# Kernel optimization log

Hardware: AMD Instinct MI355X
Metric: run time of the kernel (lower is better)

Reference implementation:

```python
import jax, jax.numpy as jnp
import numpy as np

HEADS = 16
SEQ_LEN = 2048
EMB = 1024
BATCH = 2


def setup_inputs() -> dict:
    key = jax.random.key(0)
    ks = jax.random.split(key, 5)
    s = 1.0 / np.sqrt(EMB)
    return {
        "x": jax.random.normal(ks[0], (BATCH, SEQ_LEN, EMB), dtype=jnp.float32),
        "Wk": jax.random.normal(ks[1], (EMB, EMB), dtype=jnp.float32) * s,
        "Wq": jax.random.normal(ks[2], (EMB, EMB), dtype=jnp.float32) * s,
        "Wv": jax.random.normal(ks[3], (EMB, EMB), dtype=jnp.float32) * s,
        "Wu": jax.random.normal(ks[4], (EMB, EMB), dtype=jnp.float32) * s,
        "bu": jnp.zeros((EMB,), dtype=jnp.float32),
    }


def reference(x, Wk, Wq, Wv, Wu, bu):
    B, S, E = x.shape
    H = HEADS
    D = E // H
    # projections (torch Linear: y = x @ W.T); split heads -> [B, H, S, D]
    def proj(W):
        return (x @ W.T).reshape(B, S, H, D).transpose(0, 2, 1, 3)
    q, k, v = proj(Wq), proj(Wk), proj(Wv)
    scores = jnp.einsum("bhsd,bhtd->bhst", q, k) / jnp.sqrt(jnp.float32(D))
    causal_mask = jnp.triu(jnp.ones((S, S), dtype=bool), k=1)  # True above diag
    scores = jnp.where(causal_mask, -jnp.inf, scores)
    attn = jax.nn.softmax(scores, axis=-1)
    ctx = jnp.einsum("bhst,bhtd->bhsd", attn, v)  # [B,H,S,D]
    out = ctx.transpose(0, 2, 1, 3).reshape(B, S, E)
    return out @ Wu.T + bu
```

## Files before the change

### kernel.cpp

```cpp
#include <hip/hip_runtime.h>
#include <hip/hip_bf16.h>

#define HEADS 16
#define SEQ   2048
#define EMB   1024
#define BATCH 2
#define DHEAD 64
#define MTOK  (BATCH * SEQ)

typedef __bf16 bf16x8 __attribute__((ext_vector_type(8)));
typedef float  floatx4 __attribute__((ext_vector_type(4)));

__device__ __forceinline__ void gl_lds16(const void* g, void* l) {
  __builtin_amdgcn_global_load_lds((__attribute__((address_space(1))) void*)(g),
                                   (__attribute__((address_space(3))) void*)(l), 16, 0, 0);
}

__device__ __forceinline__ unsigned short f2bf(float f) {
  __bf16 h = (__bf16)f;
  return __builtin_bit_cast(unsigned short, h);
}

__global__ __launch_bounds__(256) void cvt_kernel(
    const float* __restrict__ x,  const float* __restrict__ wq,
    const float* __restrict__ wk, const float* __restrict__ wv,
    const float* __restrict__ wu,
    unsigned short* __restrict__ xb,  unsigned short* __restrict__ wqb,
    unsigned short* __restrict__ wkb, unsigned short* __restrict__ wvb,
    unsigned short* __restrict__ wub) {
  const int g = blockIdx.x * 256 + threadIdx.x;
  const int XG = (MTOK * EMB) / 4;
  const int WG = (EMB * EMB) / 4;
  const float* src; unsigned short* dst; int off;
  if (g < XG) { src = x; dst = xb; off = g; }
  else {
    int t = g - XG; int wsel = t / WG; off = t - wsel * WG;
    const float* ss[4] = {wq, wk, wv, wu};
    unsigned short* dd[4] = {wqb, wkb, wvb, wub};
    src = ss[wsel]; dst = dd[wsel];
  }
  float4 v = ((const float4*)src)[off];
  ushort4 o;
  o.x = f2bf(v.x); o.y = f2bf(v.y); o.z = f2bf(v.z); o.w = f2bf(v.w);
  ((ushort4*)dst)[off] = o;
}

__global__ __launch_bounds__(256) void gemm_qkv(
    const unsigned short* __restrict__ xb,
    const unsigned short* __restrict__ wqb, const unsigned short* __restrict__ wkb,
    const unsigned short* __restrict__ wvb,
    unsigned short* __restrict__ Qb, unsigned short* __restrict__ Kb,
    unsigned short* __restrict__ Vt) {
  constexpr int BM = 128, BN = 64, BK = 64;
  __shared__ unsigned short As[BM * BK];
  __shared__ unsigned short Bs[3 * BN * BK];
  const int m0 = blockIdx.x * BM, n0 = blockIdx.y * BN;
  const int tid = threadIdx.x, w = tid >> 6, lane = tid & 63;
  const int quad = lane >> 4, l16 = lane & 15;
  const int wm = w >> 1, wn = w & 1;
  const int srow = lane >> 3;
  const int scol = ((lane & 7) ^ srow) * 8;
  const unsigned short* Ws[3] = {wqb, wkb, wvb};

  floatx4 acc[3][4][2] = {};

  for (int kt = 0; kt < EMB / BK; ++kt) {
    const int k0 = kt * BK;
#pragma unroll
    for (int i = 0; i < 4; ++i) {
      int r0 = i * 32 + w * 8;
      gl_lds16(xb + (size_t)(m0 + r0 + srow) * EMB + k0 + scol, &As[r0 * BK]);
    }
#pragma unroll
    for (int z = 0; z < 3; ++z)
#pragma unroll
      for (int i = 0; i < 2; ++i) {
        int r0 = i * 32 + w * 8;
        gl_lds16(Ws[z] + (size_t)(n0 + r0 + srow) * EMB + k0 + scol,
                 &Bs[z * (BN * BK) + r0 * BK]);
      }
    __syncthreads();
#pragma unroll
    for (int ks = 0; ks < 2; ++ks) {
      bf16x8 af[4];
#pragma unroll
      for (int mb = 0; mb < 4; ++mb) {
        int ra = wm * 64 + mb * 16 + l16;
        af[mb] = *(const bf16x8*)&As[ra * BK + (((ks * 4 + quad) ^ (ra & 7)) * 8)];
      }
#pragma unroll
      for (int z = 0; z < 3; ++z) {
        bf16x8 bfv[2];
#pragma unroll
        for (int nb = 0; nb < 2; ++nb) {
          int rb = wn * 32 + nb * 16 + l16;
          bfv[nb] = *(const bf16x8*)&Bs[z * (BN * BK) + rb * BK + (((ks * 4 + quad) ^ (rb & 7)) * 8)];
        }
#pragma unroll
        for (int mb = 0; mb < 4; ++mb)
#pragma unroll
          for (int nb = 0; nb < 2; ++nb)
            acc[z][mb][nb] = __builtin_amdgcn_mfma_f32_16x16x32_bf16(af[mb], bfv[nb], acc[z][mb][nb], 0, 0, 0);
      }
    }
    __syncthreads();
  }

#pragma unroll
  for (int z = 0; z < 2; ++z) {
    unsigned short* C = (z == 0) ? Qb : Kb;
    const float scale = (z == 0) ? 0.180336876f : 1.0f;
#pragma unroll
    for (int mb = 0; mb < 4; ++mb) {
#pragma unroll
      for (int nb = 0; nb < 2; ++nb) {
        int n = n0 + wn * 32 + nb * 16 + l16;
#pragma unroll
        for (int r = 0; r < 4; ++r) {
          int m = m0 + wm * 64 + mb * 16 + quad * 4 + r;
          C[(size_t)m * EMB + n] = f2bf(acc[z][mb][nb][r] * scale);
        }
      }
    }
  }
#pragma unroll
  for (int mb = 0; mb < 4; ++mb) {
    int mbase = m0 + wm * 64 + mb * 16 + quad * 4;
    int b = mbase >> 11, s = mbase & (SEQ - 1);
#pragma unroll
    for (int nb = 0; nb < 2; ++nb) {
      int n = n0 + wn * 32 + nb * 16 + l16;
      ushort4 o;
      o.x = f2bf(acc[2][mb][nb][0]); o.y = f2bf(acc[2][mb][nb][1]);
      o.z = f2bf(acc[2][mb][nb][2]); o.w = f2bf(acc[2][mb][nb][3]);
      *(ushort4*)&Vt[((size_t)b * (HEADS * DHEAD) + n) * SEQ + s] = o;
    }
  }
}

__global__ __launch_bounds__(256) void attn_kernel(
    const unsigned short* __restrict__ Qb, const unsigned short* __restrict__ Kb,
    const unsigned short* __restrict__ Vt, unsigned short* __restrict__ ctx) {
  constexpr int KT = 128;
  constexpr int PST = KT + 8;
  __shared__ unsigned short Ks[KT * DHEAD];
  __shared__ unsigned short Vs[DHEAD * KT];
  __shared__ __bf16 Ps[4 * 16 * PST];
  const int bh = blockIdx.x, pair = blockIdx.y;
  const int b = bh >> 4, h = bh & 15;
  const int tid = threadIdx.x, w = tid >> 6, lane = tid & 63;
  const int quad = lane >> 4, l16 = lane & 15;

  const unsigned short* Kbh = Kb + (size_t)b * SEQ * EMB + h * DHEAD;
  const unsigned short* Vbh = Vt + (size_t)bh * DHEAD * SEQ;
  __bf16* Pw = &Ps[w * (16 * PST)];

  int kq[4], kd[4], vd[4], vk[4];
#pragma unroll
  for (int i = 0; i < 4; ++i) {
    int c = i * 256 + tid;
    kq[i] = ((c >> 6) & 7) * 16 + (c & 15);
    kd[i] = ((c >> 9) << 5) + (((c >> 4) & 3) << 3);
    vd[i] = (((c >> 6) & 3) << 4) + (c & 15);
    vk[i] = (((c >> 8) & 3) << 5) + (((c >> 4) & 3) << 3);
  }

  for (int pi = 0; pi < 2; ++pi) {
    const int qt = pi ? (31 - pair) : pair;
    const int q0 = qt * 64;
    const int myrow = q0 + w * 16 + quad * 4;

    const size_t qrow = (size_t)(b * SEQ + q0 + w * 16 + l16) * EMB + h * DHEAD;
    bf16x8 qf[2];
    qf[0] = *(const bf16x8*)&Qb[qrow + quad * 8];
    qf[1] = *(const bf16x8*)&Qb[qrow + 32 + quad * 8];

    float lsum[4] = {0.0f, 0.0f, 0.0f, 0.0f};
    floatx4 acc_o[4] = {};

    const int nkt = (qt + 2) >> 1;
    for (int ktile = 0; ktile < nkt; ++ktile) {
      const int kt0 = ktile * KT;
#pragma unroll
      for (int i = 0; i < 4; ++i) {
        gl_lds16(Kbh + (size_t)(kt0 + kq[i]) * EMB + kd[i], &Ks[(i * 256 + w * 64) * 8]);
        gl_lds16(Vbh + (size_t)vd[i] * SEQ + kt0 + vk[i], &Vs[(i * 256 + w * 64) * 8]);
      }
      __syncthreads();

      floatx4 accs[8] = {};
#pragma unroll
      for (int ks = 0; ks < 2; ++ks)
#pragma unroll
        for (int nb = 0; nb < 8; ++nb) {
          bf16x8 kf = *(const bf16x8*)&Ks[((ks * 8 + nb) * 64 + lane) * 8];
          accs[nb] = __builtin_amdgcn_mfma_f32_16x16x32_bf16(qf[ks], kf, accs[nb], 0, 0, 0);
        }

      if (ktile == nkt - 1) {
#pragma unroll
        for (int nb = 0; nb < 8; ++nb) {
          int col = kt0 + nb * 16 + l16;
#pragma unroll
          for (int r = 0; r < 4; ++r)
            if (col > myrow + r) accs[nb][r] = -1e30f;
        }
      }

#pragma unroll
      for (int r = 0; r < 4; ++r) {
#pragma unroll
        for (int nb = 0; nb < 8; ++nb) {
          float pe = exp2f(accs[nb][r]);
          Pw[(quad * 4 + r) * PST + nb * 16 + l16] = (__bf16)pe;
          lsum[r] += pe;
        }
      }

#pragma unroll
      for (int ks = 0; ks < 4; ++ks) {
        bf16x8 pf = *(const bf16x8*)&Pw[l16 * PST + ks * 32 + quad * 8];
#pragma unroll
        for (int nb = 0; nb < 4; ++nb) {
          bf16x8 vf = *(const bf16x8*)&Vs[((ks * 4 + nb) * 64 + lane) * 8];
          acc_o[nb] = __builtin_amdgcn_mfma_f32_16x16x32_bf16(pf, vf, acc_o[nb], 0, 0, 0);
        }
      }
      __syncthreads();
    }

#pragma unroll
    for (int r = 0; r < 4; ++r) {
      float rs = lsum[r];
      rs += __shfl_xor(rs, 1);
      rs += __shfl_xor(rs, 2);
      rs += __shfl_xor(rs, 4);
      rs += __shfl_xor(rs, 8);
      float inv = 1.0f / rs;
      size_t base = (size_t)(b * SEQ + myrow + r) * EMB + h * DHEAD;
#pragma unroll
      for (int nb = 0; nb < 4; ++nb)
        ctx[base + nb * 16 + l16] = f2bf(acc_o[nb][r] * inv);
    }
  }
}

__global__ __launch_bounds__(256) void gemm_out(
    const unsigned short* __restrict__ ctx, const unsigned short* __restrict__ wub,
    const float* __restrict__ bu, float* __restrict__ out) {
  constexpr int BM = 128, BN = 64, BK = 64;
  __shared__ unsigned short As[BM * BK];
  __shared__ unsigned short Bs[BN * BK];
  const int m0 = blockIdx.x * BM, n0 = blockIdx.y * BN;
  const int tid = threadIdx.x, w = tid >> 6, lane = tid & 63;
  const int quad = lane >> 4, l16 = lane & 15;
  const int wm = w >> 1, wn = w & 1;
  const int srow = lane >> 3;
  const int scol = ((lane & 7) ^ srow) * 8;

  floatx4 acc[4][2] = {};

  for (int kt = 0; kt < EMB / BK; ++kt) {
    const int k0 = kt * BK;
#pragma unroll
    for (int i = 0; i < 4; ++i) {
      int r0 = i * 32 + w * 8;
      gl_lds16(ctx + (size_t)(m0 + r0 + srow) * EMB + k0 + scol, &As[r0 * BK]);
    }
#pragma unroll
    for (int i = 0; i < 2; ++i) {
      int r0 = i * 32 + w * 8;
      gl_lds16(wub + (size_t)(n0 + r0 + srow) * EMB + k0 + scol, &Bs[r0 * BK]);
    }
    __syncthreads();
    bf16x8 af[4][2], bfv[2][2];
#pragma unroll
    for (int mb = 0; mb < 4; ++mb) {
      int ra = wm * 64 + mb * 16 + l16;
#pragma unroll
      for (int ks = 0; ks < 2; ++ks)
        af[mb][ks] = *(const bf16x8*)&As[ra * BK + (((ks * 4 + quad) ^ (ra & 7)) * 8)];
    }
#pragma unroll
    for (int nb = 0; nb < 2; ++nb) {
      int rb = wn * 32 + nb * 16 + l16;
#pragma unroll
      for (int ks = 0; ks < 2; ++ks)
        bfv[nb][ks] = *(const bf16x8*)&Bs[rb * BK + (((ks * 4 + quad) ^ (rb & 7)) * 8)];
    }
#pragma unroll
    for (int ks = 0; ks < 2; ++ks)
#pragma unroll
      for (int mb = 0; mb < 4; ++mb)
#pragma unroll
        for (int nb = 0; nb < 2; ++nb)
          acc[mb][nb] = __builtin_amdgcn_mfma_f32_16x16x32_bf16(af[mb][ks], bfv[nb][ks], acc[mb][nb], 0, 0, 0);
    __syncthreads();
  }

#pragma unroll
  for (int mb = 0; mb < 4; ++mb) {
#pragma unroll
    for (int nb = 0; nb < 2; ++nb) {
      int n = n0 + wn * 32 + nb * 16 + l16;
      float bias = bu[n];
#pragma unroll
      for (int r = 0; r < 4; ++r) {
        int m = m0 + wm * 64 + mb * 16 + quad * 4 + r;
        out[(size_t)m * EMB + n] = acc[mb][nb][r] + bias;
      }
    }
  }
}

extern "C" void kernel_launch(void* const* d_in, const int* in_sizes, int n_in,
                              void* d_out, int out_size, void* d_ws, size_t ws_size,
                              hipStream_t stream) {
  const float* x  = (const float*)d_in[0];
  const float* Wk = (const float*)d_in[1];
  const float* Wq = (const float*)d_in[2];
  const float* Wv = (const float*)d_in[3];
  const float* Wu = (const float*)d_in[4];
  const float* bu = (const float*)d_in[5];

  char* ws = (char*)d_ws;
  const size_t MB1 = 1 << 20;
  unsigned short* xb  = (unsigned short*)(ws + 0);
  unsigned short* wqb = (unsigned short*)(ws + 8  * MB1);
  unsigned short* wkb = (unsigned short*)(ws + 10 * MB1);
  unsigned short* wvb = (unsigned short*)(ws + 12 * MB1);
  unsigned short* wub = (unsigned short*)(ws + 14 * MB1);
  unsigned short* Qb  = (unsigned short*)(ws + 16 * MB1);
  unsigned short* Kb  = (unsigned short*)(ws + 24 * MB1);
  unsigned short* Vt  = (unsigned short*)(ws + 32 * MB1);
  unsigned short* ctx = (unsigned short*)(ws + 40 * MB1);

  cvt_kernel<<<8192, 256, 0, stream>>>(x, Wq, Wk, Wv, Wu, xb, wqb, wkb, wvb, wub);
  gemm_qkv<<<dim3(32, 16), 256, 0, stream>>>(xb, wqb, wkb, wvb, Qb, Kb, Vt);
  attn_kernel<<<dim3(32, 16), 256, 0, stream>>>(Qb, Kb, Vt, ctx);
  gemm_out<<<dim3(32, 16), 256, 0, stream>>>(ctx, wub, bu, (float*)d_out);
}
```

Measured before the change: 187.6 us.

## Split attention key tiles across warps and reduce partial outputs in LDS

The attention kernel changes its work split. Before, each warp owned 16 query rows and all keys came in through shared-memory staging. Now each warp owns all 64 query rows and a 32-key slice of every 128-key tile, loading its K and V fragments straight from global memory into registers. This drops the shared K/V staging and the two block barriers per key tile. In exchange, the partial outputs and row sums are combined at the end with LDS float atomics, and there is more register pressure (launch bounds now set to 2 blocks) plus unpipelined global load latency.

```diff
diff --git a/kernel.cpp b/kernel.cpp
--- a/kernel.cpp
+++ b/kernel.cpp
@@ -138,14 +138,14 @@
   }
 }
 
-__global__ __launch_bounds__(256) void attn_kernel(
+__global__ __launch_bounds__(256, 2) void attn_kernel(
     const unsigned short* __restrict__ Qb, const unsigned short* __restrict__ Kb,
     const unsigned short* __restrict__ Vt, unsigned short* __restrict__ ctx) {
-  constexpr int KT = 128;
-  constexpr int PST = KT + 8;
-  __shared__ unsigned short Ks[KT * DHEAD];
-  __shared__ unsigned short Vs[DHEAD * KT];
-  __shared__ __bf16 Ps[4 * 16 * PST];
+  constexpr int PST = 36;
+  constexpr int OST = 68;
+  __shared__ unsigned short Ps[4 * 64 * PST];
+  __shared__ float Osum[64 * OST];
+  __shared__ float Lsum[64];
   const int bh = blockIdx.x, pair = blockIdx.y;
   const int b = bh >> 4, h = bh & 15;
   const int tid = threadIdx.x, w = tid >> 6, lane = tid & 63;
@@ -153,94 +153,124 @@
 
   const unsigned short* Kbh = Kb + (size_t)b * SEQ * EMB + h * DHEAD;
   const unsigned short* Vbh = Vt + (size_t)bh * DHEAD * SEQ;
-  __bf16* Pw = &Ps[w * (16 * PST)];
-
-  int kq[4], kd[4], vd[4], vk[4];
-#pragma unroll
-  for (int i = 0; i < 4; ++i) {
-    int c = i * 256 + tid;
-    kq[i] = ((c >> 6) & 7) * 16 + (c & 15);
-    kd[i] = ((c >> 9) << 5) + (((c >> 4) & 3) << 3);
-    vd[i] = (((c >> 6) & 3) << 4) + (c & 15);
-    vk[i] = (((c >> 8) & 3) << 5) + (((c >> 4) & 3) << 3);
-  }
+  unsigned short* Pw = &Ps[w * (64 * PST)];
+  const int kw0 = w * 32;
 
   for (int pi = 0; pi < 2; ++pi) {
     const int qt = pi ? (31 - pair) : pair;
     const int q0 = qt * 64;
-    const int myrow = q0 + w * 16 + quad * 4;
-
-    const size_t qrow = (size_t)(b * SEQ + q0 + w * 16 + l16) * EMB + h * DHEAD;
-    bf16x8 qf[2];
-    qf[0] = *(const bf16x8*)&Qb[qrow + quad * 8];
-    qf[1] = *(const bf16x8*)&Qb[qrow + 32 + quad * 8];
-
-    float lsum[4] = {0.0f, 0.0f, 0.0f, 0.0f};
-    floatx4 acc_o[4] = {};
+
+    __syncthreads();
+    for (int i = tid; i < 64 * OST; i += 256) Osum[i] = 0.0f;
+    if (tid < 64) Lsum[tid] = 0.0f;
+    __syncthreads();
+
+    bf16x8 qf[4][2];
+#pragma unroll
+    for (int mb = 0; mb < 4; ++mb) {
+      const size_t qo = (size_t)(b * SEQ + q0 + mb * 16 + l16) * EMB + h * DHEAD;
+#pragma unroll
+      for (int ks = 0; ks < 2; ++ks)
+        qf[mb][ks] = *(const bf16x8*)&Qb[qo + ks * 32 + quad * 8];
+    }
+
+    float lsum[4][4] = {};
+    floatx4 acc_o[4][4] = {};
 
     const int nkt = (qt + 2) >> 1;
-    for (int ktile = 0; ktile < nkt; ++ktile) {
-      const int kt0 = ktile * KT;
+    for (int kt = 0; kt < nkt; ++kt) {
+      const int k0 = kt * 128 + kw0;
+      bf16x8 kf[2][2], vf[4];
+#pragma unroll
+      for (int nb = 0; nb < 2; ++nb) {
+        const size_t ko = (size_t)(k0 + nb * 16 + l16) * EMB + quad * 8;
+#pragma unroll
+        for (int ks = 0; ks < 2; ++ks)
+          kf[nb][ks] = *(const bf16x8*)&Kbh[ko + ks * 32];
+      }
+#pragma unroll
+      for (int nbv = 0; nbv < 4; ++nbv)
+        vf[nbv] = *(const bf16x8*)&Vbh[(size_t)(nbv * 16 + l16) * SEQ + k0 + quad * 8];
+
+      floatx4 accs[4][2] = {};
+#pragma unroll
+      for (int ks = 0; ks < 2; ++ks)
+#pragma unroll
+        for (int mb = 0; mb < 4; ++mb)
+#pragma unroll
+          for (int nb = 0; nb < 2; ++nb)
+            accs[mb][nb] = __builtin_amdgcn_mfma_f32_16x16x32_bf16(qf[mb][ks], kf[nb][ks], accs[mb][nb], 0, 0, 0);
+
+      if (kt == nkt - 1) {
+#pragma unroll
+        for (int mb = 0; mb < 4; ++mb)
+#pragma unroll
+          for (int nb = 0; nb < 2; ++nb) {
+            int key = k0 + nb * 16 + l16;
+#pragma unroll
+            for (int r = 0; r < 4; ++r)
+              if (key > q0 + mb * 16 + quad * 4 + r) accs[mb][nb][r] = -1e30f;
+          }
+      }
+
+#pragma unroll
+      for (int mb = 0; mb < 4; ++mb)
+#pragma unroll
+        for (int r = 0; r < 4; ++r) {
+          float p0 = exp2f(accs[mb][0][r]);
+          float p1 = exp2f(accs[mb][1][r]);
+          lsum[mb][r] += p0 + p1;
+          int rowoff = (mb * 16 + quad * 4 + r) * PST + l16;
+          Pw[rowoff]      = f2bf(p0);
+          Pw[rowoff + 16] = f2bf(p1);
+        }
+
+#pragma unroll
+      for (int mb = 0; mb < 4; ++mb) {
+        bf16x8 pf = *(const bf16x8*)&Pw[(mb * 16 + l16) * PST + quad * 8];
+#pragma unroll
+        for (int nbv = 0; nbv < 4; ++nbv)
+          acc_o[mb][nbv] = __builtin_amdgcn_mfma_f32_16x16x32_bf16(pf, vf[nbv], acc_o[mb][nbv], 0, 0, 0);
+      }
+    }
+
+#pragma unroll
+    for (int mb = 0; mb < 4; ++mb)
+#pragma unroll
+      for (int nbv = 0; nbv < 4; ++nbv)
+#pragma unroll
+        for (int r = 0; r < 4; ++r)
+          atomicAdd(&Osum[(mb * 16 + quad * 4 + r) * OST + nbv * 16 + l16], acc_o[mb][nbv][r]);
+#pragma unroll
+    for (int mb = 0; mb < 4; ++mb)
+#pragma unroll
+      for (int r = 0; r < 4; ++r) {
+        float rs = lsum[mb][r];
+        rs += __shfl_xor(rs, 1);
+        rs += __shfl_xor(rs, 2);
+        rs += __shfl_xor(rs, 4);
+        rs += __shfl_xor(rs, 8);
+        if (l16 == 0) atomicAdd(&Lsum[mb * 16 + quad * 4 + r], rs);
+      }
+    __syncthreads();
+
+    {
+      const int row = w * 16 + l16;
+      const float inv = 1.0f / Lsum[row];
+      float v[16];
 #pragma unroll
       for (int i = 0; i < 4; ++i) {
-        gl_lds16(Kbh + (size_t)(kt0 + kq[i]) * EMB + kd[i], &Ks[(i * 256 + w * 64) * 8]);
-        gl_lds16(Vbh + (size_t)vd[i] * SEQ + kt0 + vk[i], &Vs[(i * 256 + w * 64) * 8]);
-      }
-      __syncthreads();
-
-      floatx4 accs[8] = {};
-#pragma unroll
-      for (int ks = 0; ks < 2; ++ks)
-#pragma unroll
-        for (int nb = 0; nb < 8; ++nb) {
-          bf16x8 kf = *(const bf16x8*)&Ks[((ks * 8 + nb) * 64 + lane) * 8];
-          accs[nb] = __builtin_amdgcn_mfma_f32_16x16x32_bf16(qf[ks], kf, accs[nb], 0, 0, 0);
-        }
-
-      if (ktile == nkt - 1) {
-#pragma unroll
-        for (int nb = 0; nb < 8; ++nb) {
-          int col = kt0 + nb * 16 + l16;
-#pragma unroll
-          for (int r = 0; r < 4; ++r)
-            if (col > myrow + r) accs[nb][r] = -1e30f;
-        }
-      }
-
-#pragma unroll
-      for (int r = 0; r < 4; ++r) {
-#pragma unroll
-        for (int nb = 0; nb < 8; ++nb) {
-          float pe = exp2f(accs[nb][r]);
-          Pw[(quad * 4 + r) * PST + nb * 16 + l16] = (__bf16)pe;
-          lsum[r] += pe;
-        }
-      }
-
-#pragma unroll
-      for (int ks = 0; ks < 4; ++ks) {
-        bf16x8 pf = *(const bf16x8*)&Pw[l16 * PST + ks * 32 + quad * 8];
-#pragma unroll
-        for (int nb = 0; nb < 4; ++nb) {
-          bf16x8 vf = *(const bf16x8*)&Vs[((ks * 4 + nb) * 64 + lane) * 8];
-          acc_o[nb] = __builtin_amdgcn_mfma_f32_16x16x32_bf16(pf, vf, acc_o[nb], 0, 0, 0);
-        }
-      }
-      __syncthreads();
-    }
-
-#pragma unroll
-    for (int r = 0; r < 4; ++r) {
-      float rs = lsum[r];
-      rs += __shfl_xor(rs, 1);
-      rs += __shfl_xor(rs, 2);
-      rs += __shfl_xor(rs, 4);
-      rs += __shfl_xor(rs, 8);
-      float inv = 1.0f / rs;
-      size_t base = (size_t)(b * SEQ + myrow + r) * EMB + h * DHEAD;
-#pragma unroll
-      for (int nb = 0; nb < 4; ++nb)
-        ctx[base + nb * 16 + l16] = f2bf(acc_o[nb][r] * inv);
+        float4 f4 = *(const float4*)&Osum[row * OST + quad * 16 + i * 4];
+        v[i * 4 + 0] = f4.x; v[i * 4 + 1] = f4.y; v[i * 4 + 2] = f4.z; v[i * 4 + 3] = f4.w;
+      }
+      unsigned short o[16];
+#pragma unroll
+      for (int i = 0; i < 16; ++i) o[i] = f2bf(v[i] * inv);
+      const size_t base = (size_t)(b * SEQ + q0 + row) * EMB + h * DHEAD + quad * 16;
+      *(ushort4*)&ctx[base]      = *(ushort4*)&o[0];
+      *(ushort4*)&ctx[base + 4]  = *(ushort4*)&o[4];
+      *(ushort4*)&ctx[base + 8]  = *(ushort4*)&o[8];
+      *(ushort4*)&ctx[base + 12] = *(ushort4*)&o[12];
     }
   }
 }
```

Result: slower. 258.7 us (+37.9%).
